# Kernel optimization log

Hardware: AMD Instinct MI355X
Metric: run time of the kernel (lower is better)

## Reference

```python
import math
import jax, jax.numpy as jnp
import numpy as np

RCR = 5.2
RCA = 3.5
ETA_R = 16.0
ETA_A = 8.0
ZETA = 32.0
NUM_SPECIES = 4
SHF_R = jnp.linspace(0.9, RCR, 17)[:-1]                      # [16]
SHF_A = jnp.linspace(0.9, RCA, 5)[:-1]                       # [4]
SHF_Z = (jnp.linspace(0.0, math.pi, 9) + math.pi / 16)[:-1]  # [8]


def _triu_index(num_species):
    i1, i2 = np.triu_indices(num_species)
    pair = np.arange(len(i1))
    ret = np.zeros((num_species, num_species), dtype=np.int32)
    ret[i1, i2] = pair
    ret[i2, i1] = pair
    return jnp.asarray(ret)

TRIU = _triu_index(NUM_SPECIES)  # [S,S] -> pair index in [0, S(S+1)/2)


def setup_inputs() -> dict:
    key = jax.random.key(0)
    k1, k2 = jax.random.split(key)
    species = jax.random.randint(k1, (64, 32), 0, NUM_SPECIES, dtype=jnp.int32)
    # spread atoms over a few Angstrom so neighbor lists are non-trivial
    coordinates = jax.random.normal(k2, (64, 32, 3), dtype=jnp.float32) * 2.0
    return {"species": species, "coordinates": coordinates}


def _cutoff_cosine(d, rc):
    # CutoffCosine: 0.5*cos(pi*d/rc)+0.5 inside cutoff, 0 outside
    return jnp.where(d <= rc, 0.5 * jnp.cos(math.pi * d / rc) + 0.5, 0.0)


def _aev(species, coordinates):
    N, A, _ = coordinates.shape
    S = NUM_SPECIES
    # vec[n,i,j] = coords[n,j] - coords[n,i]
    diff = coordinates[:, None, :, :] - coordinates[:, :, None, :]  # [N,A,A,3]
    d2 = jnp.sum(diff * diff, axis=-1)                              # [N,A,A]
    dist = jnp.sqrt(jnp.where(d2 > 0, d2, 1.0))
    eye = jnp.eye(A, dtype=bool)

    # ---- radial AEV: 0.25 * exp(-EtaR*(d-ShfR)^2) * fc(d), binned by species[j]
    rmask = (~eye) & (dist <= RCR)                                  # [N,A,A]
    fc_r = _cutoff_cosine(dist, RCR)
    g = 0.25 * jnp.exp(-ETA_R * (dist[..., None] - SHF_R) ** 2) * fc_r[..., None]
    g = g * rmask[..., None]                                        # [N,A,A,16]
    sp_onehot = jax.nn.one_hot(species, S, dtype=g.dtype)           # [N,A,S]
    radial = jnp.einsum('nijr,njs->nisr', g, sp_onehot).reshape(N, A, S * 16)

    # ---- angular AEV over triplets (i; j<k), both neighbors within Rca
    amask = (~eye) & (dist <= RCA)                                  # [N,A,A]
    fc_a = _cutoff_cosine(dist, RCA) * amask
    dot = jnp.einsum('nijc,nikc->nijk', diff, diff)                 # [N,A,A,A]
    denom = dist[:, :, :, None] * dist[:, :, None, :]
    cos_ang = jnp.clip(0.95 * dot / jnp.where(denom > 0, denom, 1.0), -0.95, 0.95)
    theta = jnp.arccos(cos_ang)                                     # [N,A,A,A]
    dmean = 0.5 * (dist[:, :, :, None] + dist[:, :, None, :])
    f1 = ((1.0 + jnp.cos(theta[..., None] - SHF_Z)) * 0.5) ** ZETA  # [N,A,A,A,8]
    f2 = jnp.exp(-ETA_A * (dmean[..., None] - SHF_A) ** 2)          # [N,A,A,A,4]
    jk = jnp.arange(A)
    tmask = amask[:, :, :, None] & amask[:, :, None, :] & (jk[:, None] < jk[None, :])
    fc_pair = fc_a[:, :, :, None] * fc_a[:, :, None, :] * tmask
    # sublength ordering: ShfA outer, ShfZ inner (EtaA, Zeta are scalars)
    term = 2.0 * f2[..., :, None] * f1[..., None, :]                # [N,A,A,A,4,8]
    term = (term * fc_pair[..., None, None]).reshape(N, A, A, A, 32)
    pair_idx = TRIU[species[:, :, None], species[:, None, :]]       # [N,A,A]
    pair_oh = jax.nn.one_hot(pair_idx, S * (S + 1) // 2, dtype=term.dtype)
    angular = jnp.einsum('nijku,njkp->nipu', term, pair_oh)
    angular = angular.reshape(N, A, (S * (S + 1) // 2) * 32)

    return jnp.concatenate([radial, angular], axis=-1)              # [N,A,384]


def reference(species, coordinates):
    aev = _aev(species, coordinates)
    return species, aev
```

## Files before the change

kernel.cpp:

```cpp
#include <hip/hip_runtime.h>
#include <math.h>

#define NATOMS 32
#define NMOL   64
#define MAXP   466
#define RCRf 5.2f
#define RCAf 3.5f

__global__ __launch_bounds__(512) void aev_kernel(const int* __restrict__ species,
                                                  const float* __restrict__ coords,
                                                  float* __restrict__ out) {
    const int bid = blockIdx.x;
    const int n = bid >> 5;
    const int i = bid & 31;
    const int tid = threadIdx.x;

    __shared__ float4 s_atom[NATOMS];
    __shared__ float2 s_dfr[NATOMS];
    __shared__ float  s_fca[NATOMS];
    __shared__ int    s_sp[NATOMS];
    __shared__ int    s_nbr[NATOMS];
    __shared__ int    s_nn;
    __shared__ __align__(16) float s_rec[MAXP*12];
    __shared__ int    s_cnt[10], s_rank[10];

    if (tid < 10) { s_cnt[tid] = 0; s_rank[tid] = 0; }
    if (tid < 64) {
        float fca_v = 0.f;
        if (tid < NATOMS) {
            const float* cb = coords + (size_t)n*NATOMS*3;
            float dx = cb[tid*3+0] - cb[i*3+0];
            float dy = cb[tid*3+1] - cb[i*3+1];
            float dz = cb[tid*3+2] - cb[i*3+2];
            float d2 = dx*dx + dy*dy + dz*dz;
            float d  = sqrtf(d2 > 0.f ? d2 : 1.f);
            bool self = (tid == i);
            float fr = (!self && d <= RCRf) ? (0.5f*__cosf(((float)M_PI/RCRf)*d) + 0.5f) : 0.f;
            fca_v    = (!self && d <= RCAf) ? (0.5f*__cosf(((float)M_PI/RCAf)*d) + 0.5f) : 0.f;
            s_atom[tid] = make_float4(dx, dy, dz, d);
            s_dfr[tid]  = make_float2(d, fr);
            s_fca[tid]  = fca_v;
            s_sp[tid]   = species[n*NATOMS + tid];
        }
        unsigned long long m = __ballot(fca_v > 0.f);
        if (fca_v > 0.f) s_nbr[__popcll(m & ((1ull << tid) - 1ull))] = tid;
        if (tid == 0) s_nn = (int)__popcll(m);
    }
    __syncthreads();

    const int nn  = s_nn;
    const int cnt = (nn*(nn-1)) >> 1;
    const int M   = 2*nn - 1;

    const float CZ[8] = { 0.98078528f,  0.83146961f,  0.55557023f,  0.19509032f,
                         -0.19509032f, -0.55557023f, -0.83146961f, -0.98078528f};
    const float SZ[8] = { 0.19509032f,  0.55557023f,  0.83146961f,  0.98078528f,
                          0.98078528f,  0.83146961f,  0.55557023f,  0.19509032f};
    const float SHA[4] = {0.9f, 1.55f, 2.2f, 2.85f};

    int px = -1;
    float4 v0, v1, v2;
    if (tid < cnt) {
        float t = sqrtf((float)(M*M - 8*tid));
        int jj = (int)(((float)M - t) * 0.5f);
        jj = max(0, min(jj, nn-2));
        while (jj*(2*nn-jj-1)/2 > tid) --jj;
        while ((jj+1)*(2*nn-jj-2)/2 <= tid) ++jj;
        int kk = tid - jj*(2*nn-jj-1)/2 + jj + 1;
        int j = s_nbr[jj], k = s_nbr[kk];
        float4 aj = s_atom[j], ak = s_atom[k];
        float fc2 = 2.f * s_fca[j] * s_fca[k];
        float dot = aj.x*ak.x + aj.y*ak.y + aj.z*ak.z;
        float c = 0.95f * dot * __builtin_amdgcn_rcpf(aj.w * ak.w);
        c = fminf(0.95f, fmaxf(-0.95f, c));
        float s = sqrtf(1.f - c*c);
        float dmean = 0.5f * (aj.w + ak.w);
        int sj = s_sp[j], sk = s_sp[k];
        int lo = min(sj, sk), hi = max(sj, sk);
        px = ((lo*(9-lo)) >> 1) + (hi - lo);
        v0.x = 0.5f + 0.5f*(c*CZ[0] + s*SZ[0]);
        v0.y = 0.5f + 0.5f*(c*CZ[1] + s*SZ[1]);
        v0.z = 0.5f + 0.5f*(c*CZ[2] + s*SZ[2]);
        v0.w = 0.5f + 0.5f*(c*CZ[3] + s*SZ[3]);
        v1.x = 0.5f + 0.5f*(c*CZ[4] + s*SZ[4]);
        v1.y = 0.5f + 0.5f*(c*CZ[5] + s*SZ[5]);
        v1.z = 0.5f + 0.5f*(c*CZ[6] + s*SZ[6]);
        v1.w = 0.5f + 0.5f*(c*CZ[7] + s*SZ[7]);
        #define POW32(q) { q = q*q; q = q*q; q = q*q; q = q*q; q = q*q; }
        POW32(v0.x) POW32(v0.y) POW32(v0.z) POW32(v0.w)
        POW32(v1.x) POW32(v1.y) POW32(v1.z) POW32(v1.w)
        #undef POW32
        float dm0 = dmean - SHA[0], dm1 = dmean - SHA[1];
        float dm2 = dmean - SHA[2], dm3 = dmean - SHA[3];
        v2.x = __expf(-8.f*dm0*dm0) * fc2;
        v2.y = __expf(-8.f*dm1*dm1) * fc2;
        v2.z = __expf(-8.f*dm2*dm2) * fc2;
        v2.w = __expf(-8.f*dm3*dm3) * fc2;
        atomicAdd(&s_cnt[px], 1);
    }
    __syncthreads();

    int c0 = s_cnt[0], c1 = s_cnt[1], c2 = s_cnt[2], c3 = s_cnt[3], c4 = s_cnt[4];
    int c5 = s_cnt[5], c6 = s_cnt[6], c7 = s_cnt[7], c8 = s_cnt[8], c9 = s_cnt[9];

    if (px >= 0) {
        int base = 0;
        base += (px > 0) ? c0 : 0;  base += (px > 1) ? c1 : 0;
        base += (px > 2) ? c2 : 0;  base += (px > 3) ? c3 : 0;
        base += (px > 4) ? c4 : 0;  base += (px > 5) ? c5 : 0;
        base += (px > 6) ? c6 : 0;  base += (px > 7) ? c7 : 0;
        base += (px > 8) ? c8 : 0;
        int slot = base + atomicAdd(&s_rank[px], 1);
        float* r = &s_rec[slot*12];
        *(float4*)(r+0) = v0;
        *(float4*)(r+4) = v1;
        *(float4*)(r+8) = v2;
    }
    __syncthreads();

    float* oa = out + NMOL*NATOMS + (size_t)bid * 384;

    if (tid < 320) {
        const int b = tid >> 5;
        const int a = (tid >> 3) & 3;
        const int z = tid & 7;
        int base = 0;
        base += (b > 0) ? c0 : 0;  base += (b > 1) ? c1 : 0;
        base += (b > 2) ? c2 : 0;  base += (b > 3) ? c3 : 0;
        base += (b > 4) ? c4 : 0;  base += (b > 5) ? c5 : 0;
        base += (b > 6) ? c6 : 0;  base += (b > 7) ? c7 : 0;
        base += (b > 8) ? c8 : 0;
        int bc = b==0?c0 : b==1?c1 : b==2?c2 : b==3?c3 : b==4?c4
               : b==5?c5 : b==6?c6 : b==7?c7 : b==8?c8 : c9;
        float acc = 0.f;
        #pragma unroll 4
        for (int q = base; q < base + bc; ++q)
            acc += s_rec[q*12 + z] * s_rec[q*12 + 8 + a];
        oa[64 + tid] = acc;
        if (tid == 0) out[bid] = (float)s_sp[i];
    } else if (tid < 384) {
        const int f  = tid - 320;
        const int rs = f >> 4;
        const float shr = 0.9f + 0.26875f * (float)(f & 15);
        float racc = 0.f;
        #pragma unroll 8
        for (int j = 0; j < NATOMS; ++j) {
            float2 dfr = s_dfr[j];
            float dmr = dfr.x - shr;
            racc += (s_sp[j] == rs) ? 0.25f * __expf(-16.f*dmr*dmr) * dfr.y : 0.f;
        }
        oa[f] = racc;
    }
}

extern "C" void kernel_launch(void* const* d_in, const int* in_sizes, int n_in,
                              void* d_out, int out_size, void* d_ws, size_t ws_size,
                              hipStream_t stream) {
    const int*   species = (const int*)d_in[0];
    const float* coords  = (const float*)d_in[1];
    float*       out     = (float*)d_out;
    aev_kernel<<<NMOL * NATOMS, 512, 0, stream>>>(species, coords, out);
}
```

Before: 16.05 us.

## Overlap radial AEV with triplet build and compact neighbor data

Moves the radial AEV computation to the top wave (threads 448-511) so it runs alongside the triplet build instead of after the final barrier. Triplet records are now built by threads 0-447, each handling up to two pairs. Neighbor coordinates, cutoff values and species are stored in compacted per-neighbor arrays so the build reads them directly rather than through an index indirection. The catch is that some threads now build two triplets, which lengthens the critical path when many pairs exist.

```diff
diff --git a/kernel.cpp b/kernel.cpp
--- a/kernel.cpp
+++ b/kernel.cpp
@@ -15,18 +15,18 @@
     const int i = bid & 31;
     const int tid = threadIdx.x;
 
-    __shared__ float4 s_atom[NATOMS];
+    __shared__ float4 s_catom[NATOMS];
+    __shared__ float2 s_cfs[NATOMS];
     __shared__ float2 s_dfr[NATOMS];
-    __shared__ float  s_fca[NATOMS];
     __shared__ int    s_sp[NATOMS];
-    __shared__ int    s_nbr[NATOMS];
     __shared__ int    s_nn;
     __shared__ __align__(16) float s_rec[MAXP*12];
     __shared__ int    s_cnt[10], s_rank[10];
 
     if (tid < 10) { s_cnt[tid] = 0; s_rank[tid] = 0; }
     if (tid < 64) {
-        float fca_v = 0.f;
+        float fca_v = 0.f, sv = 0.f;
+        float4 av;
         if (tid < NATOMS) {
             const float* cb = coords + (size_t)n*NATOMS*3;
             float dx = cb[tid*3+0] - cb[i*3+0];
@@ -37,13 +37,15 @@
             bool self = (tid == i);
             float fr = (!self && d <= RCRf) ? (0.5f*__cosf(((float)M_PI/RCRf)*d) + 0.5f) : 0.f;
             fca_v    = (!self && d <= RCAf) ? (0.5f*__cosf(((float)M_PI/RCAf)*d) + 0.5f) : 0.f;
-            s_atom[tid] = make_float4(dx, dy, dz, d);
-            s_dfr[tid]  = make_float2(d, fr);
-            s_fca[tid]  = fca_v;
-            s_sp[tid]   = species[n*NATOMS + tid];
+            int spv = species[n*NATOMS + tid];
+            s_dfr[tid] = make_float2(d, fr);
+            s_sp[tid]  = spv;
+            av = make_float4(dx, dy, dz, d);
+            sv = (float)spv;
         }
         unsigned long long m = __ballot(fca_v > 0.f);
-        if (fca_v > 0.f) s_nbr[__popcll(m & ((1ull << tid) - 1ull))] = tid;
+        int ci = (int)__popcll(m & ((1ull << tid) - 1ull));
+        if (fca_v > 0.f) { s_catom[ci] = av; s_cfs[ci] = make_float2(fca_v, sv); }
         if (tid == 0) s_nn = (int)__popcll(m);
     }
     __syncthreads();
@@ -51,6 +53,7 @@
     const int nn  = s_nn;
     const int cnt = (nn*(nn-1)) >> 1;
     const int M   = 2*nn - 1;
+    float* oa = out + NMOL*NATOMS + (size_t)bid * 384;
 
     const float CZ[8] = { 0.98078528f,  0.83146961f,  0.55557023f,  0.19509032f,
                          -0.19509032f, -0.55557023f, -0.83146961f, -0.98078528f};
@@ -58,67 +61,104 @@
                           0.98078528f,  0.83146961f,  0.55557023f,  0.19509032f};
     const float SHA[4] = {0.9f, 1.55f, 2.2f, 2.85f};
 
-    int px = -1;
-    float4 v0, v1, v2;
-    if (tid < cnt) {
-        float t = sqrtf((float)(M*M - 8*tid));
-        int jj = (int)(((float)M - t) * 0.5f);
-        jj = max(0, min(jj, nn-2));
-        while (jj*(2*nn-jj-1)/2 > tid) --jj;
-        while ((jj+1)*(2*nn-jj-2)/2 <= tid) ++jj;
-        int kk = tid - jj*(2*nn-jj-1)/2 + jj + 1;
-        int j = s_nbr[jj], k = s_nbr[kk];
-        float4 aj = s_atom[j], ak = s_atom[k];
-        float fc2 = 2.f * s_fca[j] * s_fca[k];
-        float dot = aj.x*ak.x + aj.y*ak.y + aj.z*ak.z;
-        float c = 0.95f * dot * __builtin_amdgcn_rcpf(aj.w * ak.w);
-        c = fminf(0.95f, fmaxf(-0.95f, c));
-        float s = sqrtf(1.f - c*c);
-        float dmean = 0.5f * (aj.w + ak.w);
-        int sj = s_sp[j], sk = s_sp[k];
-        int lo = min(sj, sk), hi = max(sj, sk);
-        px = ((lo*(9-lo)) >> 1) + (hi - lo);
-        v0.x = 0.5f + 0.5f*(c*CZ[0] + s*SZ[0]);
-        v0.y = 0.5f + 0.5f*(c*CZ[1] + s*SZ[1]);
-        v0.z = 0.5f + 0.5f*(c*CZ[2] + s*SZ[2]);
-        v0.w = 0.5f + 0.5f*(c*CZ[3] + s*SZ[3]);
-        v1.x = 0.5f + 0.5f*(c*CZ[4] + s*SZ[4]);
-        v1.y = 0.5f + 0.5f*(c*CZ[5] + s*SZ[5]);
-        v1.z = 0.5f + 0.5f*(c*CZ[6] + s*SZ[6]);
-        v1.w = 0.5f + 0.5f*(c*CZ[7] + s*SZ[7]);
-        #define POW32(q) { q = q*q; q = q*q; q = q*q; q = q*q; q = q*q; }
-        POW32(v0.x) POW32(v0.y) POW32(v0.z) POW32(v0.w)
-        POW32(v1.x) POW32(v1.y) POW32(v1.z) POW32(v1.w)
-        #undef POW32
-        float dm0 = dmean - SHA[0], dm1 = dmean - SHA[1];
-        float dm2 = dmean - SHA[2], dm3 = dmean - SHA[3];
-        v2.x = __expf(-8.f*dm0*dm0) * fc2;
-        v2.y = __expf(-8.f*dm1*dm1) * fc2;
-        v2.z = __expf(-8.f*dm2*dm2) * fc2;
-        v2.w = __expf(-8.f*dm3*dm3) * fc2;
-        atomicAdd(&s_cnt[px], 1);
+    if (tid >= 448) {
+        const int f  = tid - 448;
+        const int rs = f >> 4;
+        const float shr = 0.9f + 0.26875f * (float)(f & 15);
+        float racc = 0.f;
+        #pragma unroll 8
+        for (int j = 0; j < NATOMS; ++j) {
+            float2 dfr = s_dfr[j];
+            float dmr = dfr.x - shr;
+            racc += (s_sp[j] == rs) ? 0.25f * __expf(-16.f*dmr*dmr) * dfr.y : 0.f;
+        }
+        oa[f] = racc;
+        if (tid == 511) out[bid] = (float)s_sp[i];
+    }
+
+    #define BUILD(P, PX, V0, V1, V2)                                            \
+    {                                                                           \
+        float t = sqrtf((float)(M*M - 8*(P)));                                  \
+        int jj = (int)(((float)M - t) * 0.5f);                                  \
+        jj = max(0, min(jj, nn-2));                                             \
+        while (jj*(2*nn-jj-1)/2 > (P)) --jj;                                    \
+        while ((jj+1)*(2*nn-jj-2)/2 <= (P)) ++jj;                               \
+        int kk = (P) - jj*(2*nn-jj-1)/2 + jj + 1;                               \
+        float4 aj = s_catom[jj], ak = s_catom[kk];                              \
+        float2 fj = s_cfs[jj],  fk = s_cfs[kk];                                 \
+        float fc2 = 2.f * fj.x * fk.x;                                          \
+        float dot = aj.x*ak.x + aj.y*ak.y + aj.z*ak.z;                          \
+        float c = 0.95f * dot * __builtin_amdgcn_rcpf(aj.w * ak.w);             \
+        c = fminf(0.95f, fmaxf(-0.95f, c));                                     \
+        float s = sqrtf(1.f - c*c);                                             \
+        float dmean = 0.5f * (aj.w + ak.w);                                     \
+        int sj = (int)fj.y, sk = (int)fk.y;                                     \
+        int lo = min(sj, sk), hi = max(sj, sk);                                 \
+        PX = ((lo*(9-lo)) >> 1) + (hi - lo);                                    \
+        V0.x = 0.5f + 0.5f*(c*CZ[0] + s*SZ[0]);                                 \
+        V0.y = 0.5f + 0.5f*(c*CZ[1] + s*SZ[1]);                                 \
+        V0.z = 0.5f + 0.5f*(c*CZ[2] + s*SZ[2]);                                 \
+        V0.w = 0.5f + 0.5f*(c*CZ[3] + s*SZ[3]);                                 \
+        V1.x = 0.5f + 0.5f*(c*CZ[4] + s*SZ[4]);                                 \
+        V1.y = 0.5f + 0.5f*(c*CZ[5] + s*SZ[5]);                                 \
+        V1.z = 0.5f + 0.5f*(c*CZ[6] + s*SZ[6]);                                 \
+        V1.w = 0.5f + 0.5f*(c*CZ[7] + s*SZ[7]);                                 \
+        V0.x*=V0.x; V0.x*=V0.x; V0.x*=V0.x; V0.x*=V0.x; V0.x*=V0.x;            \
+        V0.y*=V0.y; V0.y*=V0.y; V0.y*=V0.y; V0.y*=V0.y; V0.y*=V0.y;            \
+        V0.z*=V0.z; V0.z*=V0.z; V0.z*=V0.z; V0.z*=V0.z; V0.z*=V0.z;            \
+        V0.w*=V0.w; V0.w*=V0.w; V0.w*=V0.w; V0.w*=V0.w; V0.w*=V0.w;            \
+        V1.x*=V1.x; V1.x*=V1.x; V1.x*=V1.x; V1.x*=V1.x; V1.x*=V1.x;            \
+        V1.y*=V1.y; V1.y*=V1.y; V1.y*=V1.y; V1.y*=V1.y; V1.y*=V1.y;            \
+        V1.z*=V1.z; V1.z*=V1.z; V1.z*=V1.z; V1.z*=V1.z; V1.z*=V1.z;            \
+        V1.w*=V1.w; V1.w*=V1.w; V1.w*=V1.w; V1.w*=V1.w; V1.w*=V1.w;            \
+        float dm0 = dmean - SHA[0], dm1 = dmean - SHA[1];                       \
+        float dm2 = dmean - SHA[2], dm3 = dmean - SHA[3];                       \
+        V2.x = __expf(-8.f*dm0*dm0) * fc2;                                      \
+        V2.y = __expf(-8.f*dm1*dm1) * fc2;                                      \
+        V2.z = __expf(-8.f*dm2*dm2) * fc2;                                      \
+        V2.w = __expf(-8.f*dm3*dm3) * fc2;                                      \
+        atomicAdd(&s_cnt[PX], 1);                                               \
+    }
+
+    int pxA = -1, pxB = -1;
+    float4 a0, a1, a2, b0, b1, b2;
+    if (tid < 448) {
+        if (tid < cnt) BUILD(tid, pxA, a0, a1, a2);
+        int p2 = tid + 448;
+        if (p2 < cnt) BUILD(p2, pxB, b0, b1, b2);
+    }
+    #undef BUILD
+    __syncthreads();
+
+    int c0=0,c1=0,c2=0,c3=0,c4=0,c5=0,c6=0,c7=0,c8=0,c9=0;
+    if (tid < 448) {
+        c0 = s_cnt[0]; c1 = s_cnt[1]; c2 = s_cnt[2]; c3 = s_cnt[3]; c4 = s_cnt[4];
+        c5 = s_cnt[5]; c6 = s_cnt[6]; c7 = s_cnt[7]; c8 = s_cnt[8]; c9 = s_cnt[9];
+    }
+
+    if (pxA >= 0) {
+        int base = 0;
+        base += (pxA > 0) ? c0 : 0;  base += (pxA > 1) ? c1 : 0;
+        base += (pxA > 2) ? c2 : 0;  base += (pxA > 3) ? c3 : 0;
+        base += (pxA > 4) ? c4 : 0;  base += (pxA > 5) ? c5 : 0;
+        base += (pxA > 6) ? c6 : 0;  base += (pxA > 7) ? c7 : 0;
+        base += (pxA > 8) ? c8 : 0;
+        int slot = base + atomicAdd(&s_rank[pxA], 1);
+        float* r = &s_rec[slot*12];
+        *(float4*)(r+0) = a0; *(float4*)(r+4) = a1; *(float4*)(r+8) = a2;
+    }
+    if (pxB >= 0) {
+        int base = 0;
+        base += (pxB > 0) ? c0 : 0;  base += (pxB > 1) ? c1 : 0;
+        base += (pxB > 2) ? c2 : 0;  base += (pxB > 3) ? c3 : 0;
+        base += (pxB > 4) ? c4 : 0;  base += (pxB > 5) ? c5 : 0;
+        base += (pxB > 6) ? c6 : 0;  base += (pxB > 7) ? c7 : 0;
+        base += (pxB > 8) ? c8 : 0;
+        int slot = base + atomicAdd(&s_rank[pxB], 1);
+        float* r = &s_rec[slot*12];
+        *(float4*)(r+0) = b0; *(float4*)(r+4) = b1; *(float4*)(r+8) = b2;
     }
     __syncthreads();
-
-    int c0 = s_cnt[0], c1 = s_cnt[1], c2 = s_cnt[2], c3 = s_cnt[3], c4 = s_cnt[4];
-    int c5 = s_cnt[5], c6 = s_cnt[6], c7 = s_cnt[7], c8 = s_cnt[8], c9 = s_cnt[9];
-
-    if (px >= 0) {
-        int base = 0;
-        base += (px > 0) ? c0 : 0;  base += (px > 1) ? c1 : 0;
-        base += (px > 2) ? c2 : 0;  base += (px > 3) ? c3 : 0;
-        base += (px > 4) ? c4 : 0;  base += (px > 5) ? c5 : 0;
-        base += (px > 6) ? c6 : 0;  base += (px > 7) ? c7 : 0;
-        base += (px > 8) ? c8 : 0;
-        int slot = base + atomicAdd(&s_rank[px], 1);
-        float* r = &s_rec[slot*12];
-        *(float4*)(r+0) = v0;
-        *(float4*)(r+4) = v1;
-        *(float4*)(r+8) = v2;
-    }
-    __syncthreads();
-
-    float* oa = out + NMOL*NATOMS + (size_t)bid * 384;
 
     if (tid < 320) {
         const int b = tid >> 5;
@@ -137,19 +177,6 @@
         for (int q = base; q < base + bc; ++q)
             acc += s_rec[q*12 + z] * s_rec[q*12 + 8 + a];
         oa[64 + tid] = acc;
-        if (tid == 0) out[bid] = (float)s_sp[i];
-    } else if (tid < 384) {
-        const int f  = tid - 320;
-        const int rs = f >> 4;
-        const float shr = 0.9f + 0.26875f * (float)(f & 15);
-        float racc = 0.f;
-        #pragma unroll 8
-        for (int j = 0; j < NATOMS; ++j) {
-            float2 dfr = s_dfr[j];
-            float dmr = dfr.x - shr;
-            racc += (s_sp[j] == rs) ? 0.25f * __expf(-16.f*dmr*dmr) * dfr.y : 0.f;
-        }
-        oa[f] = racc;
     }
 }
 
```

Result: slower. 19.89 us (+23.9%).
